# Optimization experiments

Measured on AMD Instinct MI355X. Metric: run time of the kernel, lower is better.

## Reference

```python
import jax, jax.numpy as jnp
import numpy as np

SIGMA = 0.1
B_PARAM = 1.0
EPS_NORM = 1e-12  # torch F.normalize eps
EPS_MIN = 1e-5


def setup_inputs() -> dict:
    key = jax.random.key(0)
    k1, k2 = jax.random.split(key)
    x = jax.random.normal(k1, (4, 64, 64, 64), dtype=jnp.float32)
    y = jax.random.normal(k2, (4, 64, 64, 64), dtype=jnp.float32)
    return {"x": x, "y": y}


def reference(x, y):
    B, C, H, W = x.shape
    N = H * W
    xf = x.reshape(B, C, N)
    yf = y.reshape(B, C, N)
    # F.normalize along channel dim (L2, eps-clamped denominator)
    xn = xf / jnp.maximum(jnp.linalg.norm(xf, axis=1, keepdims=True), EPS_NORM)
    yn = yf / jnp.maximum(jnp.linalg.norm(yf, axis=1, keepdims=True), EPS_NORM)
    xt = jnp.transpose(xn, (0, 2, 1))  # [B, N, C]
    yt = jnp.transpose(yn, (0, 2, 1))  # [B, N, C]
    x2 = jnp.sum(xt * xt, axis=-1, keepdims=True)          # [B, N, 1]
    y2 = jnp.sum(yt * yt, axis=-1)[:, None, :]             # [B, 1, N]
    d2 = x2 + y2 - 2.0 * jnp.einsum('bnc,bmc->bnm', xt, yt)  # [B, N, N]
    dist = jnp.sqrt(jnp.maximum(d2, 0.0))
    d_min = jnp.min(dist, axis=-1, keepdims=True)
    d_scaled = dist / (d_min + EPS_MIN)
    w = jnp.exp((B_PARAM - d_scaled) / SIGMA)
    cx = w / jnp.sum(w, axis=-1, keepdims=True)
    cx_max = jnp.max(cx, axis=-1)  # [B, N]
    return -jnp.log(jnp.mean(cx_max + EPS_MIN))
```

## Files before the change

### kernel.cpp

```cpp
#include <hip/hip_runtime.h>
#include <math.h>

constexpr int B_   = 4;
constexpr int C_   = 64;
constexpr int HW   = 4096;
constexpr int ROWS = B_ * HW;

constexpr float SIGMA    = 0.1f;
constexpr float EPS_MIN  = 1e-5f;
constexpr float EPS_NORM = 1e-12f;
constexpr float LOG2E    = 1.44269504088896340736f;

constexpr int XR  = 32;
constexpr int YW  = HW / 8;
constexpr int SRW = 32;
constexpr int NSW = YW / SRW;

using short8  = __attribute__((ext_vector_type(8))) short;
using floatx4 = __attribute__((ext_vector_type(4))) float;

__device__ inline ushort f2bf(float f) {
    unsigned u = __float_as_uint(f);
    unsigned r = u + 0x7FFFu + ((u >> 16) & 1u);
    return (ushort)(r >> 16);
}

__global__ __launch_bounds__(256) void nrm_kernel(const float* __restrict__ x,
                                                  const float* __restrict__ y,
                                                  ushort* __restrict__ xn,
                                                  ushort* __restrict__ yn,
                                                  float* __restrict__ total) {
    int p = blockIdx.x * 256 + threadIdx.x;
    if (p == 0) *total = 0.0f;
    const float* src; ushort* dst; int q;
    if (p < ROWS) { src = x; dst = xn; q = p; }
    else          { src = y; dst = yn; q = p - ROWS; }
    int b = q >> 12;
    int n = q & (HW - 1);
    const float* base = src + ((size_t)b * C_) * HW + n;
    float v[C_];
    float ss = 0.0f;
#pragma unroll
    for (int c = 0; c < C_; ++c) {
        v[c] = base[(size_t)c * HW];
        ss = fmaf(v[c], v[c], ss);
    }
    float scale = 1.0f / fmaxf(sqrtf(ss), EPS_NORM);
    short8* o = (short8*)(dst + (size_t)q * C_);
#pragma unroll
    for (int c8 = 0; c8 < C_ / 8; ++c8) {
        short8 pk;
#pragma unroll
        for (int j = 0; j < 8; ++j) pk[j] = (short)f2bf(v[c8 * 8 + j] * scale);
        o[c8] = pk;
    }
}

__global__ __launch_bounds__(512, 4) void main_kernel(const ushort* __restrict__ xn,
                                                      const ushort* __restrict__ yn,
                                                      float* __restrict__ total) {
    __shared__ short8 stg[8][2][SRW * 8];
    __shared__ float  red[8][XR];
    __shared__ float  dmf[XR];

    const int tid  = threadIdx.x;
    const int wid  = tid >> 6;
    const int lane = tid & 63;
    const int lrow = lane & 15;
    const int kgrp = lane >> 4;

    const int blk   = blockIdx.x;
    const int b     = blk >> 7;
    const int nbase = (blk & 127) * XR;

    const ushort* xb = xn + (size_t)(b * HW + nbase) * C_;
    short8 xf0[2], xf1[2];
#pragma unroll
    for (int xt = 0; xt < 2; ++xt) {
        xf0[xt] = *(const short8*)(xb + (xt * 16 + lrow) * C_ + kgrp * 8);
        xf1[xt] = *(const short8*)(xb + (xt * 16 + lrow) * C_ + 32 + kgrp * 8);
    }

    const short8* yq = (const short8*)(yn + (size_t)(b * HW + wid * YW) * C_);
    const int wbase = (lane >> 3) * 8 + ((lane & 7) ^ (lane >> 3));

    short8 v[4];
    float st0[2] = {-INFINITY, -INFINITY};

#pragma unroll
    for (int g = 0; g < 4; ++g) v[g] = yq[g * 64 + lane];
#pragma unroll
    for (int g = 0; g < 4; ++g) stg[wid][0][g * 64 + wbase] = v[g];

    for (int s = 0; s < NSW; ++s) {
        int cur = s & 1;
        if (s + 1 < NSW) {
#pragma unroll
            for (int g = 0; g < 4; ++g) v[g] = yq[(s + 1) * 256 + g * 64 + lane];
        }
#pragma unroll
        for (int yt = 0; yt < 2; ++yt) {
            int p = yt * 16 + lrow, q = p & 7;
            short8 ya0 = stg[wid][cur][p * 8 + (kgrp ^ q)];
            short8 ya1 = stg[wid][cur][p * 8 + ((kgrp + 4) ^ q)];
#pragma unroll
            for (int xt = 0; xt < 2; ++xt) {
                floatx4 acc = {0.0f, 0.0f, 0.0f, 0.0f};
                acc = __builtin_amdgcn_mfma_f32_16x16x32_bf16(ya0, xf0[xt], acc, 0, 0, 0);
                acc = __builtin_amdgcn_mfma_f32_16x16x32_bf16(ya1, xf1[xt], acc, 0, 0, 0);
                st0[xt] = fmaxf(st0[xt],
                          fmaxf(fmaxf(acc[0], acc[1]), fmaxf(acc[2], acc[3])));
            }
        }
        if (s + 1 < NSW) {
#pragma unroll
            for (int g = 0; g < 4; ++g) stg[wid][cur ^ 1][g * 64 + wbase] = v[g];
        }
    }

#pragma unroll
    for (int off = 16; off < 64; off <<= 1) {
        st0[0] = fmaxf(st0[0], __shfl_xor(st0[0], off));
        st0[1] = fmaxf(st0[1], __shfl_xor(st0[1], off));
    }
    if (kgrp == 0) { red[wid][lrow] = st0[0]; red[wid][16 + lrow] = st0[1]; }
    __syncthreads();
    if (tid < XR) {
        float m = red[0][tid];
#pragma unroll
        for (int w = 1; w < 8; ++w) m = fmaxf(m, red[w][tid]);
        dmf[tid] = sqrtf(fmaxf(fmaf(-2.0f, m, 2.0f), 0.0f));
    }
    __syncthreads();

    float kk2[2], c02[2];
#pragma unroll
    for (int xt = 0; xt < 2; ++xt) {
        float dm = dmf[xt * 16 + lrow];
        kk2[xt] = LOG2E / (SIGMA * (dm + EPS_MIN));
        c02[xt] = dm * kk2[xt];
    }

    float s2[2] = {0.0f, 0.0f};
#pragma unroll
    for (int g = 0; g < 4; ++g) v[g] = yq[g * 64 + lane];
#pragma unroll
    for (int g = 0; g < 4; ++g) stg[wid][0][g * 64 + wbase] = v[g];

    for (int s = 0; s < NSW; ++s) {
        int cur = s & 1;
        if (s + 1 < NSW) {
#pragma unroll
            for (int g = 0; g < 4; ++g) v[g] = yq[(s + 1) * 256 + g * 64 + lane];
        }
#pragma unroll
        for (int yt = 0; yt < 2; ++yt) {
            int p = yt * 16 + lrow, q = p & 7;
            short8 ya0 = stg[wid][cur][p * 8 + (kgrp ^ q)];
            short8 ya1 = stg[wid][cur][p * 8 + ((kgrp + 4) ^ q)];
#pragma unroll
            for (int xt = 0; xt < 2; ++xt) {
                floatx4 acc = {0.0f, 0.0f, 0.0f, 0.0f};
                acc = __builtin_amdgcn_mfma_f32_16x16x32_bf16(ya0, xf0[xt], acc, 0, 0, 0);
                acc = __builtin_amdgcn_mfma_f32_16x16x32_bf16(ya1, xf1[xt], acc, 0, 0, 0);
#pragma unroll
                for (int r = 0; r < 4; ++r) {
                    float d2 = fmaxf(fmaf(-2.0f, acc[r], 2.0f), 0.0f);
                    float d  = __builtin_amdgcn_sqrtf(d2);
                    s2[xt] += __builtin_amdgcn_exp2f(fmaf(-kk2[xt], d, c02[xt]));
                }
            }
        }
        if (s + 1 < NSW) {
#pragma unroll
            for (int g = 0; g < 4; ++g) stg[wid][cur ^ 1][g * 64 + wbase] = v[g];
        }
    }

#pragma unroll
    for (int off = 16; off < 64; off <<= 1) {
        s2[0] += __shfl_xor(s2[0], off);
        s2[1] += __shfl_xor(s2[1], off);
    }
    if (kgrp == 0) { red[wid][lrow] = s2[0]; red[wid][16 + lrow] = s2[1]; }
    __syncthreads();

    if (tid < 64) {
        float acc = 0.0f;
        if (tid < XR) {
            float Ssum = red[0][tid];
#pragma unroll
            for (int w = 1; w < 8; ++w) Ssum += red[w][tid];
            acc = __builtin_amdgcn_rcpf(Ssum) + EPS_MIN;
        }
#pragma unroll
        for (int off = 16; off > 0; off >>= 1) acc += __shfl_down(acc, off);
        if (tid == 0) atomicAdd(total, acc);
    }
}

__global__ void final_kernel(const float* __restrict__ total,
                             float* __restrict__ out) {
    out[0] = -logf(total[0] / (float)ROWS);
}

extern "C" void kernel_launch(void* const* d_in, const int* in_sizes, int n_in,
                              void* d_out, int out_size, void* d_ws, size_t ws_size,
                              hipStream_t stream) {
    const float* x = (const float*)d_in[0];
    const float* y = (const float*)d_in[1];
    float* out = (float*)d_out;

    char* ws = (char*)d_ws;
    size_t nrm_bytes = (size_t)ROWS * C_ * sizeof(ushort);
    ushort* xn    = (ushort*)(ws);
    ushort* yn    = (ushort*)(ws + nrm_bytes);
    float*  total = (float*)(ws + 2 * nrm_bytes);

    hipLaunchKernelGGL(nrm_kernel, dim3(2 * ROWS / 256), dim3(256), 0, stream,
                       x, y, xn, yn, total);
    hipLaunchKernelGGL(main_kernel, dim3(ROWS / XR), dim3(512), 0, stream,
                       xn, yn, total);
    hipLaunchKernelGGL(final_kernel, dim3(1), dim3(1), 0, stream, total, out);
}
```

Baseline: 99.03 us.

## Load Y fragments directly from global and fold distance affine into MFMA

Removes the LDS staging buffer for Y tiles. Each lane now loads its MFMA fragments straight from global/L2 with two-tile register prefetching. The normalization kernel pre-scales x by -2, and accumulators are seeded with 2.0, so the MFMA output is already the squared distance. This removes the per-element fma/max before the sqrt and turns the max search into a min search. The cost is more uncoalesced-ish global loads and the loss of the clamp at zero, so tiny negative rounding values could reach the sqrt.

```diff
diff --git a/kernel.cpp b/kernel.cpp
--- a/kernel.cpp
+++ b/kernel.cpp
@@ -11,13 +11,15 @@
 constexpr float EPS_NORM = 1e-12f;
 constexpr float LOG2E    = 1.44269504088896340736f;
 
-constexpr int XR  = 32;
-constexpr int YW  = HW / 8;
-constexpr int SRW = 32;
-constexpr int NSW = YW / SRW;
+constexpr int XR = 32;
+constexpr int NW = 8;
+constexpr int YW = HW / NW;
+constexpr int NT = YW / 16;
 
 using short8  = __attribute__((ext_vector_type(8))) short;
 using floatx4 = __attribute__((ext_vector_type(4))) float;
+
+struct Frag { short8 a0, a1; };
 
 __device__ inline ushort f2bf(float f) {
     unsigned u = __float_as_uint(f);
@@ -32,9 +34,9 @@
                                                   float* __restrict__ total) {
     int p = blockIdx.x * 256 + threadIdx.x;
     if (p == 0) *total = 0.0f;
-    const float* src; ushort* dst; int q;
-    if (p < ROWS) { src = x; dst = xn; q = p; }
-    else          { src = y; dst = yn; q = p - ROWS; }
+    const float* src; ushort* dst; int q; float sgn;
+    if (p < ROWS) { src = x; dst = xn; q = p; sgn = -2.0f; }
+    else          { src = y; dst = yn; q = p - ROWS; sgn = 1.0f; }
     int b = q >> 12;
     int n = q & (HW - 1);
     const float* base = src + ((size_t)b * C_) * HW + n;
@@ -45,7 +47,7 @@
         v[c] = base[(size_t)c * HW];
         ss = fmaf(v[c], v[c], ss);
     }
-    float scale = 1.0f / fmaxf(sqrtf(ss), EPS_NORM);
+    float scale = sgn / fmaxf(sqrtf(ss), EPS_NORM);
     short8* o = (short8*)(dst + (size_t)q * C_);
 #pragma unroll
     for (int c8 = 0; c8 < C_ / 8; ++c8) {
@@ -59,9 +61,8 @@
 __global__ __launch_bounds__(512, 4) void main_kernel(const ushort* __restrict__ xn,
                                                       const ushort* __restrict__ yn,
                                                       float* __restrict__ total) {
-    __shared__ short8 stg[8][2][SRW * 8];
-    __shared__ float  red[8][XR];
-    __shared__ float  dmf[XR];
+    __shared__ float red[NW][XR];
+    __shared__ float dmf[XR];
 
     const int tid  = threadIdx.x;
     const int wid  = tid >> 6;
@@ -81,55 +82,50 @@
         xf1[xt] = *(const short8*)(xb + (xt * 16 + lrow) * C_ + 32 + kgrp * 8);
     }
 
-    const short8* yq = (const short8*)(yn + (size_t)(b * HW + wid * YW) * C_);
-    const int wbase = (lane >> 3) * 8 + ((lane & 7) ^ (lane >> 3));
-
-    short8 v[4];
-    float st0[2] = {-INFINITY, -INFINITY};
-
-#pragma unroll
-    for (int g = 0; g < 4; ++g) v[g] = yq[g * 64 + lane];
-#pragma unroll
-    for (int g = 0; g < 4; ++g) stg[wid][0][g * 64 + wbase] = v[g];
-
-    for (int s = 0; s < NSW; ++s) {
-        int cur = s & 1;
-        if (s + 1 < NSW) {
-#pragma unroll
-            for (int g = 0; g < 4; ++g) v[g] = yq[(s + 1) * 256 + g * 64 + lane];
+    const ushort* lb = yn + (size_t)(b * HW + wid * YW + lrow) * C_ + kgrp * 8;
+
+#define LDT(t) Frag{ *(const short8*)(lb + (t) * 16 * C_), \
+                     *(const short8*)(lb + (t) * 16 * C_ + 32) }
+
+    float m2[2] = {INFINITY, INFINITY};
+    {
+        Frag fa = LDT(0), fb = LDT(1);
+        for (int t = 0; t < NT; t += 2) {
+            Frag fc = {}, fd = {};
+            if (t + 2 < NT) fc = LDT(t + 2);
+            if (t + 3 < NT) fd = LDT(t + 3);
+#pragma unroll
+            for (int xt = 0; xt < 2; ++xt) {
+                floatx4 acc = {2.0f, 2.0f, 2.0f, 2.0f};
+                acc = __builtin_amdgcn_mfma_f32_16x16x32_bf16(fa.a0, xf0[xt], acc, 0, 0, 0);
+                acc = __builtin_amdgcn_mfma_f32_16x16x32_bf16(fa.a1, xf1[xt], acc, 0, 0, 0);
+                m2[xt] = fminf(m2[xt],
+                         fminf(fminf(acc[0], acc[1]), fminf(acc[2], acc[3])));
+            }
+#pragma unroll
+            for (int xt = 0; xt < 2; ++xt) {
+                floatx4 acc = {2.0f, 2.0f, 2.0f, 2.0f};
+                acc = __builtin_amdgcn_mfma_f32_16x16x32_bf16(fb.a0, xf0[xt], acc, 0, 0, 0);
+                acc = __builtin_amdgcn_mfma_f32_16x16x32_bf16(fb.a1, xf1[xt], acc, 0, 0, 0);
+                m2[xt] = fminf(m2[xt],
+                         fminf(fminf(acc[0], acc[1]), fminf(acc[2], acc[3])));
+            }
+            fa = fc; fb = fd;
         }
-#pragma unroll
-        for (int yt = 0; yt < 2; ++yt) {
-            int p = yt * 16 + lrow, q = p & 7;
-            short8 ya0 = stg[wid][cur][p * 8 + (kgrp ^ q)];
-            short8 ya1 = stg[wid][cur][p * 8 + ((kgrp + 4) ^ q)];
-#pragma unroll
-            for (int xt = 0; xt < 2; ++xt) {
-                floatx4 acc = {0.0f, 0.0f, 0.0f, 0.0f};
-                acc = __builtin_amdgcn_mfma_f32_16x16x32_bf16(ya0, xf0[xt], acc, 0, 0, 0);
-                acc = __builtin_amdgcn_mfma_f32_16x16x32_bf16(ya1, xf1[xt], acc, 0, 0, 0);
-                st0[xt] = fmaxf(st0[xt],
-                          fmaxf(fmaxf(acc[0], acc[1]), fmaxf(acc[2], acc[3])));
-            }
-        }
-        if (s + 1 < NSW) {
-#pragma unroll
-            for (int g = 0; g < 4; ++g) stg[wid][cur ^ 1][g * 64 + wbase] = v[g];
-        }
     }
 
 #pragma unroll
     for (int off = 16; off < 64; off <<= 1) {
-        st0[0] = fmaxf(st0[0], __shfl_xor(st0[0], off));
-        st0[1] = fmaxf(st0[1], __shfl_xor(st0[1], off));
-    }
-    if (kgrp == 0) { red[wid][lrow] = st0[0]; red[wid][16 + lrow] = st0[1]; }
+        m2[0] = fminf(m2[0], __shfl_xor(m2[0], off));
+        m2[1] = fminf(m2[1], __shfl_xor(m2[1], off));
+    }
+    if (kgrp == 0) { red[wid][lrow] = m2[0]; red[wid][16 + lrow] = m2[1]; }
     __syncthreads();
     if (tid < XR) {
         float m = red[0][tid];
 #pragma unroll
-        for (int w = 1; w < 8; ++w) m = fmaxf(m, red[w][tid]);
-        dmf[tid] = sqrtf(fmaxf(fmaf(-2.0f, m, 2.0f), 0.0f));
+        for (int w = 1; w < NW; ++w) m = fminf(m, red[w][tid]);
+        dmf[tid] = sqrtf(fmaxf(m, 0.0f));
     }
     __syncthreads();
 
@@ -142,40 +138,38 @@
     }
 
     float s2[2] = {0.0f, 0.0f};
-#pragma unroll
-    for (int g = 0; g < 4; ++g) v[g] = yq[g * 64 + lane];
-#pragma unroll
-    for (int g = 0; g < 4; ++g) stg[wid][0][g * 64 + wbase] = v[g];
-
-    for (int s = 0; s < NSW; ++s) {
-        int cur = s & 1;
-        if (s + 1 < NSW) {
-#pragma unroll
-            for (int g = 0; g < 4; ++g) v[g] = yq[(s + 1) * 256 + g * 64 + lane];
-        }
-#pragma unroll
-        for (int yt = 0; yt < 2; ++yt) {
-            int p = yt * 16 + lrow, q = p & 7;
-            short8 ya0 = stg[wid][cur][p * 8 + (kgrp ^ q)];
-            short8 ya1 = stg[wid][cur][p * 8 + ((kgrp + 4) ^ q)];
-#pragma unroll
-            for (int xt = 0; xt < 2; ++xt) {
-                floatx4 acc = {0.0f, 0.0f, 0.0f, 0.0f};
-                acc = __builtin_amdgcn_mfma_f32_16x16x32_bf16(ya0, xf0[xt], acc, 0, 0, 0);
-                acc = __builtin_amdgcn_mfma_f32_16x16x32_bf16(ya1, xf1[xt], acc, 0, 0, 0);
+    {
+        Frag fa = LDT(0), fb = LDT(1);
+        for (int t = 0; t < NT; t += 2) {
+            Frag fc = {}, fd = {};
+            if (t + 2 < NT) fc = LDT(t + 2);
+            if (t + 3 < NT) fd = LDT(t + 3);
+#pragma unroll
+            for (int xt = 0; xt < 2; ++xt) {
+                floatx4 acc = {2.0f, 2.0f, 2.0f, 2.0f};
+                acc = __builtin_amdgcn_mfma_f32_16x16x32_bf16(fa.a0, xf0[xt], acc, 0, 0, 0);
+                acc = __builtin_amdgcn_mfma_f32_16x16x32_bf16(fa.a1, xf1[xt], acc, 0, 0, 0);
 #pragma unroll
                 for (int r = 0; r < 4; ++r) {
-                    float d2 = fmaxf(fmaf(-2.0f, acc[r], 2.0f), 0.0f);
-                    float d  = __builtin_amdgcn_sqrtf(d2);
+                    float d = __builtin_amdgcn_sqrtf(acc[r]);
                     s2[xt] += __builtin_amdgcn_exp2f(fmaf(-kk2[xt], d, c02[xt]));
                 }
             }
+#pragma unroll
+            for (int xt = 0; xt < 2; ++xt) {
+                floatx4 acc = {2.0f, 2.0f, 2.0f, 2.0f};
+                acc = __builtin_amdgcn_mfma_f32_16x16x32_bf16(fb.a0, xf0[xt], acc, 0, 0, 0);
+                acc = __builtin_amdgcn_mfma_f32_16x16x32_bf16(fb.a1, xf1[xt], acc, 0, 0, 0);
+#pragma unroll
+                for (int r = 0; r < 4; ++r) {
+                    float d = __builtin_amdgcn_sqrtf(acc[r]);
+                    s2[xt] += __builtin_amdgcn_exp2f(fmaf(-kk2[xt], d, c02[xt]));
+                }
+            }
+            fa = fc; fb = fd;
         }
-        if (s + 1 < NSW) {
-#pragma unroll
-            for (int g = 0; g < 4; ++g) stg[wid][cur ^ 1][g * 64 + wbase] = v[g];
-        }
-    }
+    }
+#undef LDT
 
 #pragma unroll
     for (int off = 16; off < 64; off <<= 1) {
@@ -190,7 +184,7 @@
         if (tid < XR) {
             float Ssum = red[0][tid];
 #pragma unroll
-            for (int w = 1; w < 8; ++w) Ssum += red[w][tid];
+            for (int w = 1; w < NW; ++w) Ssum += red[w][tid];
             acc = __builtin_amdgcn_rcpf(Ssum) + EPS_MIN;
         }
 #pragma unroll
```

Measured after the change: 127.4 us. 1.29x slower.

## Double rows per block with 16 waves and fold distance affine into MFMA

Applied to the files above, without the earlier changes.

Each block now handles 64 x rows with 16 waves of 1024 threads. Each wave sweeps 256 y columns against 4 x tiles, so every staged y fragment in LDS is reused twice as often. The normalization pre-scales x by -2 and the MFMA accumulator starts at 2, so it directly yields squared distance and the per-element fma and clamp are dropped. The risks are that dropping the clamp lets slightly negative bf16 rounding values reach sqrt, and that the larger blocks with more registers may lower occupancy.

```diff
diff --git a/kernel.cpp b/kernel.cpp
--- a/kernel.cpp
+++ b/kernel.cpp
@@ -11,8 +11,9 @@
 constexpr float EPS_NORM = 1e-12f;
 constexpr float LOG2E    = 1.44269504088896340736f;
 
-constexpr int XR  = 32;
-constexpr int YW  = HW / 8;
+constexpr int XR  = 64;
+constexpr int NW  = 16;
+constexpr int YW  = HW / NW;
 constexpr int SRW = 32;
 constexpr int NSW = YW / SRW;
 
@@ -32,9 +33,9 @@
                                                   float* __restrict__ total) {
     int p = blockIdx.x * 256 + threadIdx.x;
     if (p == 0) *total = 0.0f;
-    const float* src; ushort* dst; int q;
-    if (p < ROWS) { src = x; dst = xn; q = p; }
-    else          { src = y; dst = yn; q = p - ROWS; }
+    const float* src; ushort* dst; int q; float sgn;
+    if (p < ROWS) { src = x; dst = xn; q = p; sgn = -2.0f; }
+    else          { src = y; dst = yn; q = p - ROWS; sgn = 1.0f; }
     int b = q >> 12;
     int n = q & (HW - 1);
     const float* base = src + ((size_t)b * C_) * HW + n;
@@ -45,7 +46,7 @@
         v[c] = base[(size_t)c * HW];
         ss = fmaf(v[c], v[c], ss);
     }
-    float scale = 1.0f / fmaxf(sqrtf(ss), EPS_NORM);
+    float scale = sgn / fmaxf(sqrtf(ss), EPS_NORM);
     short8* o = (short8*)(dst + (size_t)q * C_);
 #pragma unroll
     for (int c8 = 0; c8 < C_ / 8; ++c8) {
@@ -56,11 +57,11 @@
     }
 }
 
-__global__ __launch_bounds__(512, 4) void main_kernel(const ushort* __restrict__ xn,
-                                                      const ushort* __restrict__ yn,
-                                                      float* __restrict__ total) {
-    __shared__ short8 stg[8][2][SRW * 8];
-    __shared__ float  red[8][XR];
+__global__ __launch_bounds__(1024, 4) void main_kernel(const ushort* __restrict__ xn,
+                                                       const ushort* __restrict__ yn,
+                                                       float* __restrict__ total) {
+    __shared__ short8 stg[NW][2][SRW * 8];
+    __shared__ float  red[NW][XR];
     __shared__ float  dmf[XR];
 
     const int tid  = threadIdx.x;
@@ -70,13 +71,13 @@
     const int kgrp = lane >> 4;
 
     const int blk   = blockIdx.x;
-    const int b     = blk >> 7;
-    const int nbase = (blk & 127) * XR;
+    const int b     = blk >> 6;
+    const int nbase = (blk & 63) * XR;
 
     const ushort* xb = xn + (size_t)(b * HW + nbase) * C_;
-    short8 xf0[2], xf1[2];
-#pragma unroll
-    for (int xt = 0; xt < 2; ++xt) {
+    short8 xf0[4], xf1[4];
+#pragma unroll
+    for (int xt = 0; xt < 4; ++xt) {
         xf0[xt] = *(const short8*)(xb + (xt * 16 + lrow) * C_ + kgrp * 8);
         xf1[xt] = *(const short8*)(xb + (xt * 16 + lrow) * C_ + 32 + kgrp * 8);
     }
@@ -85,7 +86,7 @@
     const int wbase = (lane >> 3) * 8 + ((lane & 7) ^ (lane >> 3));
 
     short8 v[4];
-    float st0[2] = {-INFINITY, -INFINITY};
+    float m2[4] = {INFINITY, INFINITY, INFINITY, INFINITY};
 
 #pragma unroll
     for (int g = 0; g < 4; ++g) v[g] = yq[g * 64 + lane];
@@ -104,12 +105,12 @@
             short8 ya0 = stg[wid][cur][p * 8 + (kgrp ^ q)];
             short8 ya1 = stg[wid][cur][p * 8 + ((kgrp + 4) ^ q)];
 #pragma unroll
-            for (int xt = 0; xt < 2; ++xt) {
-                floatx4 acc = {0.0f, 0.0f, 0.0f, 0.0f};
+            for (int xt = 0; xt < 4; ++xt) {
+                floatx4 acc = {2.0f, 2.0f, 2.0f, 2.0f};
                 acc = __builtin_amdgcn_mfma_f32_16x16x32_bf16(ya0, xf0[xt], acc, 0, 0, 0);
                 acc = __builtin_amdgcn_mfma_f32_16x16x32_bf16(ya1, xf1[xt], acc, 0, 0, 0);
-                st0[xt] = fmaxf(st0[xt],
-                          fmaxf(fmaxf(acc[0], acc[1]), fmaxf(acc[2], acc[3])));
+                m2[xt] = fminf(m2[xt],
+                         fminf(fminf(acc[0], acc[1]), fminf(acc[2], acc[3])));
             }
         }
         if (s + 1 < NSW) {
@@ -119,29 +120,31 @@
     }
 
 #pragma unroll
-    for (int off = 16; off < 64; off <<= 1) {
-        st0[0] = fmaxf(st0[0], __shfl_xor(st0[0], off));
-        st0[1] = fmaxf(st0[1], __shfl_xor(st0[1], off));
-    }
-    if (kgrp == 0) { red[wid][lrow] = st0[0]; red[wid][16 + lrow] = st0[1]; }
+    for (int off = 16; off < 64; off <<= 1)
+#pragma unroll
+        for (int xt = 0; xt < 4; ++xt)
+            m2[xt] = fminf(m2[xt], __shfl_xor(m2[xt], off));
+    if (kgrp == 0)
+#pragma unroll
+        for (int xt = 0; xt < 4; ++xt) red[wid][xt * 16 + lrow] = m2[xt];
     __syncthreads();
     if (tid < XR) {
         float m = red[0][tid];
 #pragma unroll
-        for (int w = 1; w < 8; ++w) m = fmaxf(m, red[w][tid]);
-        dmf[tid] = sqrtf(fmaxf(fmaf(-2.0f, m, 2.0f), 0.0f));
+        for (int w = 1; w < NW; ++w) m = fminf(m, red[w][tid]);
+        dmf[tid] = sqrtf(fmaxf(m, 0.0f));
     }
     __syncthreads();
 
-    float kk2[2], c02[2];
-#pragma unroll
-    for (int xt = 0; xt < 2; ++xt) {
+    float kk2[4], c02[4];
+#pragma unroll
+    for (int xt = 0; xt < 4; ++xt) {
         float dm = dmf[xt * 16 + lrow];
         kk2[xt] = LOG2E / (SIGMA * (dm + EPS_MIN));
         c02[xt] = dm * kk2[xt];
     }
 
-    float s2[2] = {0.0f, 0.0f};
+    float s2[4] = {0.0f, 0.0f, 0.0f, 0.0f};
 #pragma unroll
     for (int g = 0; g < 4; ++g) v[g] = yq[g * 64 + lane];
 #pragma unroll
@@ -159,14 +162,13 @@
             short8 ya0 = stg[wid][cur][p * 8 + (kgrp ^ q)];
             short8 ya1 = stg[wid][cur][p * 8 + ((kgrp + 4) ^ q)];
 #pragma unroll
-            for (int xt = 0; xt < 2; ++xt) {
-                floatx4 acc = {0.0f, 0.0f, 0.0f, 0.0f};
+            for (int xt = 0; xt < 4; ++xt) {
+                floatx4 acc = {2.0f, 2.0f, 2.0f, 2.0f};
                 acc = __builtin_amdgcn_mfma_f32_16x16x32_bf16(ya0, xf0[xt], acc, 0, 0, 0);
                 acc = __builtin_amdgcn_mfma_f32_16x16x32_bf16(ya1, xf1[xt], acc, 0, 0, 0);
 #pragma unroll
                 for (int r = 0; r < 4; ++r) {
-                    float d2 = fmaxf(fmaf(-2.0f, acc[r], 2.0f), 0.0f);
-                    float d  = __builtin_amdgcn_sqrtf(d2);
+                    float d = __builtin_amdgcn_sqrtf(acc[r]);
                     s2[xt] += __builtin_amdgcn_exp2f(fmaf(-kk2[xt], d, c02[xt]));
                 }
             }
@@ -178,23 +180,22 @@
     }
 
 #pragma unroll
-    for (int off = 16; off < 64; off <<= 1) {
-        s2[0] += __shfl_xor(s2[0], off);
-        s2[1] += __shfl_xor(s2[1], off);
-    }
-    if (kgrp == 0) { red[wid][lrow] = s2[0]; red[wid][16 + lrow] = s2[1]; }
+    for (int off = 16; off < 64; off <<= 1)
+#pragma unroll
+        for (int xt = 0; xt < 4; ++xt)
+            s2[xt] += __shfl_xor(s2[xt], off);
+    if (kgrp == 0)
+#pragma unroll
+        for (int xt = 0; xt < 4; ++xt) red[wid][xt * 16 + lrow] = s2[xt];
     __syncthreads();
 
     if (tid < 64) {
-        float acc = 0.0f;
-        if (tid < XR) {
-            float Ssum = red[0][tid];
-#pragma unroll
-            for (int w = 1; w < 8; ++w) Ssum += red[w][tid];
-            acc = __builtin_amdgcn_rcpf(Ssum) + EPS_MIN;
-        }
-#pragma unroll
-        for (int off = 16; off > 0; off >>= 1) acc += __shfl_down(acc, off);
+        float Ssum = red[0][tid];
+#pragma unroll
+        for (int w = 1; w < NW; ++w) Ssum += red[w][tid];
+        float acc = __builtin_amdgcn_rcpf(Ssum) + EPS_MIN;
+#pragma unroll
+        for (int off = 32; off > 0; off >>= 1) acc += __shfl_down(acc, off);
         if (tid == 0) atomicAdd(total, acc);
     }
 }
@@ -219,7 +220,7 @@
 
     hipLaunchKernelGGL(nrm_kernel, dim3(2 * ROWS / 256), dim3(256), 0, stream,
                        x, y, xn, yn, total);
-    hipLaunchKernelGGL(main_kernel, dim3(ROWS / XR), dim3(512), 0, stream,
+    hipLaunchKernelGGL(main_kernel, dim3(ROWS / XR), dim3(1024), 0, stream,
                        xn, yn, total);
     hipLaunchKernelGGL(final_kernel, dim3(1), dim3(1), 0, stream, total, out);
 }
```

Measured after the change: 93.29 us. -5.8%, faster.
